# Optimization experiments

Measured on AMD Instinct MI355X. Metric: run time of the kernel, lower is better.

Reference implementation:

```python
import jax, jax.numpy as jnp
import numpy as np

N_NODES = 100000
N_EDGES = 1600000
IN_F = 256
OUT_F = 128


def setup_inputs() -> dict:
    key = jax.random.key(0)
    k1, k2, k3, k4, k5, k6 = jax.random.split(key, 6)
    x = jax.random.normal(k1, (N_NODES, IN_F), dtype=jnp.float32)
    stdv = 1.0 / np.sqrt(OUT_F)
    weight = jax.random.uniform(k2, (IN_F, OUT_F), dtype=jnp.float32, minval=-stdv, maxval=stdv)
    bias = jax.random.uniform(k3, (OUT_F,), dtype=jnp.float32, minval=-stdv, maxval=stdv)
    edge_src = jax.random.randint(k4, (N_EDGES,), 0, N_NODES, dtype=jnp.int32)
    edge_dst = jnp.sort(jax.random.randint(k5, (N_EDGES,), 0, N_NODES, dtype=jnp.int32))
    edge_val = jax.random.uniform(k6, (N_EDGES,), dtype=jnp.float32)
    return {"x": x, "weight": weight, "bias": bias,
            "edge_src": edge_src, "edge_dst": edge_dst, "edge_val": edge_val}


def reference(x, weight, bias, edge_src, edge_dst, edge_val):
    # support = X @ W   (dense GEMM, [N, out_f])
    support = x @ weight
    # output = A @ support, A sparse COO: out[dst] += val * support[src]
    msgs = support[edge_src] * edge_val[:, None]          # [E, out_f]
    output = jax.ops.segment_sum(msgs, edge_dst, num_segments=N_NODES,
                                 indices_are_sorted=True)  # [N, out_f]
    return jnp.tanh(output + bias)
```

## Files before the change

kernel.cpp:

```cpp
#include <hip/hip_runtime.h>
#include <hip/hip_bf16.h>

typedef _Float16 f16;
typedef f16 f16x8 __attribute__((ext_vector_type(8)));
typedef f16 f16x4 __attribute__((ext_vector_type(4)));
typedef f16 f16x2 __attribute__((ext_vector_type(2)));
typedef float f32x4 __attribute__((ext_vector_type(4)));

#define IN_F 256
#define OUT_F 128
#define BK 64

__global__ __launch_bounds__(256) void prep_w(const float* __restrict__ W,
                                              f16* __restrict__ Wt) {
    int i = blockIdx.x * 256 + threadIdx.x;
    int k = i >> 7;
    int n = i & 127;
    Wt[n * IN_F + k] = (f16)W[i];
}

__global__ __launch_bounds__(256) void seg_bounds(const int* __restrict__ dst,
                                                  int* __restrict__ rs,
                                                  int* __restrict__ re, int E) {
    int i = blockIdx.x * 256 + threadIdx.x;
    if (i >= E) return;
    int d = dst[i];
    if (i == 0 || dst[i - 1] != d) rs[d] = i;
    if (i == E - 1 || dst[i + 1] != d) re[d] = i + 1;
}

__global__ __launch_bounds__(256) void gemm_xw(const float* __restrict__ X,
                                               const f16* __restrict__ Wt,
                                               f16* __restrict__ S, int M) {
    __shared__ f16 sx[2][128 * BK] __attribute__((aligned(16)));

    const int w   = threadIdx.x >> 6;
    const int l   = threadIdx.x & 63;
    const int r   = l & 15;
    const int khi = l >> 4;
    const int wm = w >> 1, wn = w & 1;
    const int brow  = blockIdx.x * 128;
    const int mbase = wm * 64;
    const int nbase = wn * 64;

    const int srow = w * 32 + (l >> 4);
    const int scol = (l & 15) * 4;

    f32x4 acc[4][4] = {};
    float4 xv[8];

    #pragma unroll
    for (int j = 0; j < 8; ++j) {
        int rloc = srow + j * 4;
        int rg = brow + rloc; rg = rg < M ? rg : M - 1;
        xv[j] = *(const float4*)(X + (size_t)rg * IN_F + scol);
    }
    #pragma unroll
    for (int j = 0; j < 8; ++j) {
        int rloc = srow + j * 4;
        f16x4 hv = { (f16)xv[j].x, (f16)xv[j].y, (f16)xv[j].z, (f16)xv[j].w };
        *(f16x4*)&sx[0][rloc * BK + (scol ^ ((rloc & 7) << 3))] = hv;
    }
    __syncthreads();

    #pragma unroll
    for (int t = 0; t < 4; ++t) {
        if (t < 3) {
            const int k0 = (t + 1) * BK;
            #pragma unroll
            for (int j = 0; j < 8; ++j) {
                int rloc = srow + j * 4;
                int rg = brow + rloc; rg = rg < M ? rg : M - 1;
                xv[j] = *(const float4*)(X + (size_t)rg * IN_F + k0 + scol);
            }
        }
        #pragma unroll
        for (int kk = 0; kk < 2; ++kk) {
            f16x8 a[4], b[4];
            const int sidx = (kk * 32 + khi * 8) ^ ((r & 7) << 3);
            #pragma unroll
            for (int m = 0; m < 4; ++m) {
                int arow = mbase + m * 16 + r;
                a[m] = *(const f16x8*)&sx[t & 1][arow * BK + sidx];
            }
            const int kg = t * BK + kk * 32 + khi * 8;
            #pragma unroll
            for (int n = 0; n < 4; ++n)
                b[n] = *(const f16x8*)(Wt + (size_t)(nbase + n * 16 + r) * IN_F + kg);
            #pragma unroll
            for (int m = 0; m < 4; ++m)
                #pragma unroll
                for (int n = 0; n < 4; ++n)
                    acc[m][n] = __builtin_amdgcn_mfma_f32_16x16x32_f16(a[m], b[n], acc[m][n], 0, 0, 0);
        }
        if (t < 3) {
            #pragma unroll
            for (int j = 0; j < 8; ++j) {
                int rloc = srow + j * 4;
                f16x4 hv = { (f16)xv[j].x, (f16)xv[j].y, (f16)xv[j].z, (f16)xv[j].w };
                *(f16x4*)&sx[(t + 1) & 1][rloc * BK + (scol ^ ((rloc & 7) << 3))] = hv;
            }
        }
        __syncthreads();
    }

    #pragma unroll
    for (int m = 0; m < 4; ++m) {
        int row0 = brow + mbase + m * 16 + khi * 4;
        #pragma unroll
        for (int i = 0; i < 4; ++i) {
            int row = row0 + i;
            if (row < M) {
                #pragma unroll
                for (int n = 0; n < 4; ++n)
                    S[(size_t)row * OUT_F + nbase + n * 16 + r] = (f16)acc[m][n][i];
            }
        }
    }
}

__global__ __launch_bounds__(256) void aggregate(const f16* __restrict__ S,
                                                 const int* __restrict__ rs,
                                                 const int* __restrict__ re,
                                                 const int* __restrict__ esrc,
                                                 const float* __restrict__ eval,
                                                 const float* __restrict__ bias,
                                                 float* __restrict__ out, int N) {
    const int wave = threadIdx.x >> 6;
    const int lane = threadIdx.x & 63;
    const int node = blockIdx.x * 4 + wave;
    if (node >= N) return;

    const int g = lane >> 4;
    const int p = lane & 15;

    const int s = rs[node];
    const int e = re[node];

    float acc[8] = {};

    for (int base = s; base < e; base += 16) {
        int   se[4];
        float ve[4];
        #pragma unroll
        for (int j = 0; j < 4; ++j) {
            int ei  = base + j * 4 + g;
            int eic = min(ei, e - 1);
            se[j] = esrc[eic];
            ve[j] = eval[eic];
            if (ei >= e) ve[j] = 0.f;
        }
        f16x8 h[4];
        #pragma unroll
        for (int j = 0; j < 4; ++j)
            h[j] = *(const f16x8*)(S + (size_t)se[j] * OUT_F + p * 8);
        #pragma unroll
        for (int j = 0; j < 4; ++j)
            #pragma unroll
            for (int q = 0; q < 8; ++q)
                acc[q] += ve[j] * (float)h[j][q];
    }

    #pragma unroll
    for (int q = 0; q < 8; ++q) {
        acc[q] += __shfl_xor(acc[q], 16);
        acc[q] += __shfl_xor(acc[q], 32);
    }

    if (lane < 32) {
        const int half = lane >> 4;
        const int f0 = 8 * p + 4 * half;
        float4 bb = *(const float4*)(bias + f0);
        float4 o;
        o.x = tanhf(acc[4 * half + 0] + bb.x);
        o.y = tanhf(acc[4 * half + 1] + bb.y);
        o.z = tanhf(acc[4 * half + 2] + bb.z);
        o.w = tanhf(acc[4 * half + 3] + bb.w);
        *(float4*)(out + (size_t)node * OUT_F + f0) = o;
    }
}

extern "C" void kernel_launch(void* const* d_in, const int* in_sizes, int n_in,
                              void* d_out, int out_size, void* d_ws, size_t ws_size,
                              hipStream_t stream) {
    const float* X    = (const float*)d_in[0];
    const float* W    = (const float*)d_in[1];
    const float* bias = (const float*)d_in[2];
    const int*   esrc = (const int*)d_in[3];
    const int*   edst = (const int*)d_in[4];
    const float* eval = (const float*)d_in[5];
    float* out = (float*)d_out;

    const int N = in_sizes[0] / IN_F;
    const int E = in_sizes[3];

    char* ws = (char*)d_ws;
    f16* Wt = (f16*)ws;
    f16* S  = (f16*)(ws + 65536);
    int* rs = (int*)(ws + 65536 + (size_t)N * OUT_F * 2);
    int* re = rs + N;

    hipMemsetAsync(rs, 0, 2 * (size_t)N * sizeof(int), stream);
    prep_w<<<(IN_F * OUT_F) / 256, 256, 0, stream>>>(W, Wt);
    seg_bounds<<<(E + 255) / 256, 256, 0, stream>>>(edst, rs, re, E);
    gemm_xw<<<(N + 127) / 128, 256, 0, stream>>>(X, Wt, S, N);
    aggregate<<<(N + 3) / 4, 256, 0, stream>>>(S, rs, re, esrc, eval, bias, out, N);
}
```

Before: 114.4 us.

## Store GEMM output in feature slabs and aggregate one slab per pass

The GEMM now writes S in a slab-major layout, with 16 features per slab stored contiguously across all nodes. The aggregation kernel splits the feature dimension into 8 passes, one per block group. Each half-wave handles one node and gathers only 32-byte slab rows, so each pass's working set of S (about 3.2 MB) is small enough to stay cache-resident. The cost is that edge indices and values are re-read 8 times, and there are more shuffle reductions and more blocks.

```diff
diff --git a/kernel.cpp b/kernel.cpp
--- a/kernel.cpp
+++ b/kernel.cpp
@@ -4,7 +4,6 @@
 typedef _Float16 f16;
 typedef f16 f16x8 __attribute__((ext_vector_type(8)));
 typedef f16 f16x4 __attribute__((ext_vector_type(4)));
-typedef f16 f16x2 __attribute__((ext_vector_type(2)));
 typedef float f32x4 __attribute__((ext_vector_type(4)));
 
 #define IN_F 256
@@ -112,8 +111,10 @@
             int row = row0 + i;
             if (row < M) {
                 #pragma unroll
-                for (int n = 0; n < 4; ++n)
-                    S[(size_t)row * OUT_F + nbase + n * 16 + r] = (f16)acc[m][n][i];
+                for (int n = 0; n < 4; ++n) {
+                    int slab = (nbase >> 4) + n;
+                    S[((size_t)slab * M + row) * 16 + r] = (f16)acc[m][n][i];
+                }
             }
         }
     }
@@ -126,57 +127,53 @@
                                                  const float* __restrict__ eval,
                                                  const float* __restrict__ bias,
                                                  float* __restrict__ out, int N) {
-    const int wave = threadIdx.x >> 6;
-    const int lane = threadIdx.x & 63;
-    const int node = blockIdx.x * 4 + wave;
+    const int pass = blockIdx.x & 7;
+    const int node = (blockIdx.x >> 3) * 8 + (threadIdx.x >> 5);
     if (node >= N) return;
 
-    const int g = lane >> 4;
-    const int p = lane & 15;
+    const int hl   = threadIdx.x & 31;
+    const int slot = hl >> 1;
+    const int half = hl & 1;
 
     const int s = rs[node];
     const int e = re[node];
 
+    const f16* Sp = S + (size_t)pass * N * 16 + half * 8;
+
     float acc[8] = {};
 
     for (int base = s; base < e; base += 16) {
-        int   se[4];
-        float ve[4];
+        int ei  = base + slot;
+        int eic = min(ei, e - 1);
+        int   se = __builtin_nontemporal_load(esrc + eic);
+        float ve = __builtin_nontemporal_load(eval + eic);
+        if (ei >= e) ve = 0.f;
+        f16x8 h = *(const f16x8*)(Sp + (size_t)se * 16);
         #pragma unroll
-        for (int j = 0; j < 4; ++j) {
-            int ei  = base + j * 4 + g;
-            int eic = min(ei, e - 1);
-            se[j] = esrc[eic];
-            ve[j] = eval[eic];
-            if (ei >= e) ve[j] = 0.f;
-        }
-        f16x8 h[4];
-        #pragma unroll
-        for (int j = 0; j < 4; ++j)
-            h[j] = *(const f16x8*)(S + (size_t)se[j] * OUT_F + p * 8);
-        #pragma unroll
-        for (int j = 0; j < 4; ++j)
-            #pragma unroll
-            for (int q = 0; q < 8; ++q)
-                acc[q] += ve[j] * (float)h[j][q];
+        for (int q = 0; q < 8; ++q)
+            acc[q] += ve * (float)h[q];
     }
 
     #pragma unroll
     for (int q = 0; q < 8; ++q) {
+        acc[q] += __shfl_xor(acc[q], 2);
+        acc[q] += __shfl_xor(acc[q], 4);
+        acc[q] += __shfl_xor(acc[q], 8);
         acc[q] += __shfl_xor(acc[q], 16);
-        acc[q] += __shfl_xor(acc[q], 32);
-    }
-
-    if (lane < 32) {
-        const int half = lane >> 4;
-        const int f0 = 8 * p + 4 * half;
-        float4 bb = *(const float4*)(bias + f0);
-        float4 o;
-        o.x = tanhf(acc[4 * half + 0] + bb.x);
-        o.y = tanhf(acc[4 * half + 1] + bb.y);
-        o.z = tanhf(acc[4 * half + 2] + bb.z);
-        o.w = tanhf(acc[4 * half + 3] + bb.w);
-        *(float4*)(out + (size_t)node * OUT_F + f0) = o;
+    }
+
+    if (hl < 2) {
+        const int f0 = pass * 16 + half * 8;
+        float4 b0 = *(const float4*)(bias + f0);
+        float4 b1 = *(const float4*)(bias + f0 + 4);
+        float4 o0, o1;
+        o0.x = tanhf(acc[0] + b0.x); o0.y = tanhf(acc[1] + b0.y);
+        o0.z = tanhf(acc[2] + b0.z); o0.w = tanhf(acc[3] + b0.w);
+        o1.x = tanhf(acc[4] + b1.x); o1.y = tanhf(acc[5] + b1.y);
+        o1.z = tanhf(acc[6] + b1.z); o1.w = tanhf(acc[7] + b1.w);
+        float* op = out + (size_t)node * OUT_F + f0;
+        *(float4*)op = o0;
+        *(float4*)(op + 4) = o1;
     }
 }
 
@@ -204,5 +201,6 @@
     prep_w<<<(IN_F * OUT_F) / 256, 256, 0, stream>>>(W, Wt);
     seg_bounds<<<(E + 255) / 256, 256, 0, stream>>>(edst, rs, re, E);
     gemm_xw<<<(N + 127) / 128, 256, 0, stream>>>(X, Wt, S, N);
-    aggregate<<<(N + 3) / 4, 256, 0, stream>>>(S, rs, re, esrc, eval, bias, out, N);
-}
+    const int ngroups = (N + 7) / 8;
+    aggregate<<<ngroups * 8, 256, 0, stream>>>(S, rs, re, esrc, eval, bias, out, N);
+}
```

Result: slower. 287.6 us (+151.5%).
